# Performance work log

Hardware: AMD Instinct MI355X
Metric: run time of the kernel (lower is better)

The kernel has to match this reference:

```python
import jax, jax.numpy as jnp
import numpy as np

EPS = float(np.finfo(np.float32).eps)
FFT_SIZE, HOP, WIN = 1024, 120, 600
ANCHOR, KF = 7, 7
LRELU_SLOPE = 0.1

def make_log_shift(anchor=ANCHOR, kf=KF, out_scale=1000.0, in_scale=0.001):
    s = (np.arange(kf) + 1) / anchor
    ls = out_scale * np.log(in_scale * s)
    ls -= ls[anchor - 1]
    return -ls  # positive, monotonically decreasing to 0 at the anchor tap

SHIFTS = make_log_shift()

def stft_mag(y):
    # y: (B, T) -> (B, 513, n_frames), matches torch.stft(center=True, reflect)
    B, T = y.shape
    pad = FFT_SIZE // 2
    yp = jnp.pad(y, ((0, 0), (pad, pad)), mode='reflect')
    n_frames = 1 + (T + 2 * pad - FFT_SIZE) // HOP
    idx = jnp.arange(n_frames)[:, None] * HOP + jnp.arange(FFT_SIZE)[None, :]
    frames = yp[:, idx]                                  # (B, n_frames, fft)
    n = np.arange(WIN)
    w = 0.5 * (1.0 - np.cos(2.0 * np.pi * n / WIN))      # periodic Hann(600)
    lp = (FFT_SIZE - WIN) // 2                           # centered pad to fft
    w = jnp.asarray(np.pad(w, (lp, FFT_SIZE - WIN - lp)), dtype=y.dtype)
    spec = jnp.fft.rfft(frames * w, axis=-1)
    mag = jnp.sqrt(jnp.clip(spec.real ** 2 + spec.imag ** 2, EPS))
    return jnp.transpose(mag, (0, 2, 1))

def int_shift(x, k):
    # output[..., f, :] = x[..., f-k, :], zero-fill; k >= 0 (static python int)
    F = x.shape[2]
    if k == 0:
        return x
    if k >= F:
        return jnp.zeros_like(x)
    return jnp.pad(x[:, :, :F - k, :], ((0, 0), (0, 0), (k, 0), (0, 0)))

def frac_shift(x, s):
    # linear-interpolation frequency shift (= interp_shift CUDA kernel)
    if s == int(s):
        return int_shift(x, int(s))
    s0 = int(np.floor(s)); frac = float(s - s0)
    return (1.0 - frac) * int_shift(x, s0) + frac * int_shift(x, s0 + 1)

def wnorm(v, g):
    # weight_norm: w = g * v / ||v|| (norm over all dims but out-channel)
    n = jnp.sqrt(jnp.sum(v * v, axis=(1, 2, 3), keepdims=True))
    return g * v / n

def conv2d(x, w, b, stride, padding):
    out = jax.lax.conv_general_dilated(
        x, w, window_strides=stride,
        padding=((padding[0], padding[0]), (padding[1], padding[1])),
        dimension_numbers=('NCHW', 'OIHW', 'NCHW'))
    return out + b[None, :, None, None]

def lrelu(x):
    return jax.nn.leaky_relu(x, LRELU_SLOPE)

def harmonic_conv(x, v, g, b):
    # x: (B,1,F,T). Log-harmonic lowering: stack 7 fractionally-shifted copies
    lowered = jnp.concatenate([frac_shift(x, SHIFTS[fk]) for fk in range(KF)], axis=1)
    w = wnorm(v, g)                                      # (32, 7, 1, 7)
    return conv2d(lowered, w, b, (1, 1), (0, 3))         # padding[0] forced to 0

def setup_inputs() -> dict:
    key = jax.random.key(0)
    ks = jax.random.split(key, 16)
    p = {}
    p['y'] = jax.random.normal(ks[0], (4, 1, 96000), dtype=jnp.float32)
    p['v0'] = jax.random.normal(ks[1], (32, 7, 1, 7), dtype=jnp.float32) * 0.05
    p['g0'] = jnp.ones((32, 1, 1, 1), dtype=jnp.float32)
    p['b0'] = jnp.zeros((32,), dtype=jnp.float32)
    for i, kk in zip((1, 2, 3), (2, 3, 4)):
        p[f'v{i}'] = jax.random.normal(ks[kk], (32, 32, 3, 9), dtype=jnp.float32) * 0.05
        p[f'g{i}'] = jnp.ones((32, 1, 1, 1), dtype=jnp.float32)
        p[f'b{i}'] = jnp.zeros((32,), dtype=jnp.float32)
    p['v4'] = jax.random.normal(ks[5], (32, 32, 3, 3), dtype=jnp.float32) * 0.05
    p['g4'] = jnp.ones((32, 1, 1, 1), dtype=jnp.float32)
    p['b4'] = jnp.zeros((32,), dtype=jnp.float32)
    p['vo'] = jax.random.normal(ks[6], (1, 32, 3, 3), dtype=jnp.float32) * 0.05
    p['go'] = jnp.ones((1, 1, 1, 1), dtype=jnp.float32)
    p['bo'] = jnp.zeros((1,), dtype=jnp.float32)
    return p

def reference(y, v0, g0, b0, v1, g1, b1, v2, g2, b2, v3, g3, b3,
              v4, g4, b4, vo, go, bo):
    mag = stft_mag(y[:, 0, :])          # (B, 513, frames)
    x = mag[:, None]                    # (B, 1, 513, frames)
    fmap = []
    x = lrelu(harmonic_conv(x, v0, g0, b0)); fmap.append(x)
    x = lrelu(conv2d(x, wnorm(v1, g1), b1, (1, 2), (1, 4))); fmap.append(x)
    x = lrelu(conv2d(x, wnorm(v2, g2), b2, (1, 2), (1, 4))); fmap.append(x)
    x = lrelu(conv2d(x, wnorm(v3, g3), b3, (1, 2), (1, 4))); fmap.append(x)
    x = lrelu(conv2d(x, wnorm(v4, g4), b4, (1, 1), (1, 1))); fmap.append(x)
    x = conv2d(x, wnorm(vo, go), bo, (1, 1), (1, 1)); fmap.append(x)
    flat = x.reshape(x.shape[0], -1)
    return (flat,) + tuple(fmap)
```

## Files before the change

kernel.cpp:

```cpp
#include <hip/hip_runtime.h>
#include <math.h>

#define T_SAMPLES 96000
#define NFRAMES 801
#define NBINS 513
#define FROWS 515
#define MAGT 804
#define EPS32 1.1920928955078125e-07f

typedef _Float16 f16;
typedef f16 f16x2 __attribute__((ext_vector_type(2)));
typedef f16 f16x4 __attribute__((ext_vector_type(4)));
typedef f16 f16x8 __attribute__((ext_vector_type(8)));
typedef float f32x4 __attribute__((ext_vector_type(4)));
typedef float f32x16 __attribute__((ext_vector_type(16)));

__global__ __launch_bounds__(256) void stft_v2(const float* __restrict__ y,
                                               float* __restrict__ mag)
{
    __shared__ float2 fft[2][4][1024];
    float* mg = (float*)&fft[1][0][0];
    const int MGS = 520;

    const int tid  = threadIdx.x;
    const int lane = tid & 63;
    const int wv   = tid >> 6;
    const int t0   = blockIdx.x * 8;
    const int b    = blockIdx.y;
    const float* yb = y + (size_t)b * T_SAMPLES;

    const int tA = t0 + 2 * wv;
    for (int n = lane; n < 1024; n += 64) {
        float w = 0.f;
        int np_ = n - 212;
        if (np_ >= 0 && np_ < 600)
            w = 0.5f * (1.0f - cospif((float)np_ * (1.0f / 300.0f)));
        int j1 = tA * 120 + n - 512;
        if (j1 < 0) j1 = -j1;
        if (j1 >= T_SAMPLES) j1 = 2 * T_SAMPLES - 2 - j1;
        int j2 = j1 + 120;
        {
            int jj = tA * 120 + 120 + n - 512;
            if (jj < 0) jj = -jj;
            if (jj >= T_SAMPLES) jj = 2 * T_SAMPLES - 2 - jj;
            j2 = jj;
        }
        fft[0][wv][n] = make_float2(w * yb[j1], w * yb[j2]);
    }
    __syncthreads();

    int srcb = 0;
    #pragma unroll
    for (int stage = 0; stage < 10; ++stage) {
        int m = 1 << stage;
        #pragma unroll
        for (int it = 0; it < 8; ++it) {
            int idx = lane + it * 64;
            int jm  = (idx >> stage) << stage;
            float jf = (float)jm * (1.0f / 512.0f);
            float wr = cospif(jf);
            float wi = -sinpif(jf);
            float2 a  = fft[srcb][wv][idx];
            float2 bb = fft[srcb][wv][idx + 512];
            float2 s  = make_float2(a.x + bb.x, a.y + bb.y);
            float2 d  = make_float2(a.x - bb.x, a.y - bb.y);
            float2 dw = make_float2(d.x * wr - d.y * wi, d.x * wi + d.y * wr);
            fft[srcb ^ 1][wv][idx + jm]     = s;
            fft[srcb ^ 1][wv][idx + jm + m] = dw;
        }
        __syncthreads();
        srcb ^= 1;
    }

    for (int k = lane; k < 513; k += 64) {
        float2 zk = fft[0][wv][k];
        float2 zr = fft[0][wv][(1024 - k) & 1023];
        float x1r = 0.5f * (zk.x + zr.x);
        float x1i = 0.5f * (zk.y - zr.y);
        float x2r = 0.5f * (zk.y + zr.y);
        float x2i = 0.5f * (zr.x - zk.x);
        mg[(2 * wv)     * MGS + k] = sqrtf(fmaxf(x1r * x1r + x1i * x1i, EPS32));
        mg[(2 * wv + 1) * MGS + k] = sqrtf(fmaxf(x2r * x2r + x2i * x2i, EPS32));
    }
    __syncthreads();

    for (int f = tid; f < 513; f += 256) {
        size_t base = ((size_t)(b * NBINS) + f) * MAGT + t0;
        if (t0 + 7 < NFRAMES) {
            f32x4 v0 = {mg[0 * MGS + f], mg[1 * MGS + f], mg[2 * MGS + f], mg[3 * MGS + f]};
            f32x4 v1 = {mg[4 * MGS + f], mg[5 * MGS + f], mg[6 * MGS + f], mg[7 * MGS + f]};
            *reinterpret_cast<f32x4*>(&mag[base])     = v0;
            *reinterpret_cast<f32x4*>(&mag[base + 4]) = v1;
        } else {
            #pragma unroll
            for (int p = 0; p < 8; ++p)
                if (t0 + p < NFRAMES) mag[base + p] = mg[p * MGS + f];
        }
    }
}

__global__ __launch_bounds__(256) void prep_kernel(
    const float* __restrict__ v0, const float* __restrict__ g0,
    const float* __restrict__ v1, const float* __restrict__ g1,
    const float* __restrict__ v2, const float* __restrict__ g2,
    const float* __restrict__ v3, const float* __restrict__ g3,
    const float* __restrict__ v4, const float* __restrict__ g4,
    const float* __restrict__ vo, const float* __restrict__ go,
    float* __restrict__ w0n, float* __restrict__ won,
    f16* __restrict__ A1, f16* __restrict__ A2,
    f16* __restrict__ A3, f16* __restrict__ A4,
    f16* __restrict__ f0c, f16* __restrict__ f1c, f16* __restrict__ f2c,
    f16* __restrict__ f3c, f16* __restrict__ f4c)
{
    int blk = blockIdx.x;
    int tid = threadIdx.x;

    if (blk >= 161) {
        int zb = blk - 161;
        const int TPs[5]   = {840, 456, 264, 136, 136};
        const int tails[5] = {840, 420, 228, 133, 136};
        f16* ptrs[5] = {f0c, f1c, f2c, f3c, f4c};
        f16x8 z;
        #pragma unroll
        for (int j = 0; j < 8; ++j) z[j] = (f16)0.f;
        for (int l = 0; l < 5; ++l) {
            f16* p = ptrs[l];
            int TP = TPs[l], tail = tails[l];
            int rowSlots   = TP * 4;
            int guardSlots = 8 * rowSlots;
            int tailCols   = TP - tail;
            int tailSlots  = 4 * FROWS * tailCols * 4;
            int total = guardSlots + tailSlots;
            for (int i = zb * 256 + tid; i < total; i += 256 * 256) {
                size_t slot;
                if (i < guardSlots) {
                    int rs = i / rowSlots;
                    int q  = i - rs * rowSlots;
                    int b  = rs >> 1;
                    int r  = (rs & 1) ? (FROWS - 1) : 0;
                    slot = ((size_t)(b * FROWS + r)) * rowSlots + q;
                } else {
                    int j2 = i - guardSlots;
                    int per = tailCols * 4;
                    int row = j2 / per;
                    int q   = j2 - row * per;
                    slot = ((size_t)row * TP + tail) * 4 + q;
                }
                *reinterpret_cast<f16x8*>((char*)p + slot * 16) = z;
            }
        }
        return;
    }

    const float *v, *g; f16* Ap = nullptr; float* outf = nullptr;
    int o, per_o, KW = 9;
    if (blk < 32)        { v = v1; g = g1; Ap = A1; o = blk;       per_o = 864; }
    else if (blk < 64)   { v = v2; g = g2; Ap = A2; o = blk - 32;  per_o = 864; }
    else if (blk < 96)   { v = v3; g = g3; Ap = A3; o = blk - 64;  per_o = 864; }
    else if (blk < 128)  { v = v4; g = g4; Ap = A4; o = blk - 96;  per_o = 288; KW = 3; }
    else if (blk < 160)  { v = v0; g = g0; outf = w0n; o = blk - 128; per_o = 49; }
    else                 { v = vo; g = go; outf = won; o = 0;        per_o = 288; }

    const float* vv = v + (size_t)o * per_o;
    __shared__ float red[256];
    float s = 0.f;
    for (int i = tid; i < per_o; i += 256) { float x = vv[i]; s = fmaf(x, x, s); }
    red[tid] = s;
    __syncthreads();
    for (int k = 128; k > 0; k >>= 1) {
        if (tid < k) red[tid] += red[tid + k];
        __syncthreads();
    }
    float scale = g[o] / sqrtf(red[0]);

    if (outf) {
        for (int i = tid; i < per_o; i += 256)
            outf[(size_t)o * per_o + i] = vv[i] * scale;
    } else {
        for (int i = tid; i < per_o; i += 256) {
            int tap = i >> 5;
            int c   = i & 31;
            int df  = tap / KW, kw = tap - df * KW;
            float val = vv[(c * 3 + df) * KW + kw] * scale;
            int l = ((c >> 3) & 1) * 32 + o;
            int ch = c >> 4;
            int j = c & 7;
            Ap[(((tap * 2 + ch) * 64 + l) << 3) + j] = (f16)val;
        }
    }
}

__global__ __launch_bounds__(256) void harmonic_kernel(const float* __restrict__ mag,
                                                       const float* __restrict__ wn,
                                                       const float* __restrict__ bias,
                                                       float* __restrict__ out,
                                                       f16* __restrict__ f0c,
                                                       float fr4, float fr5)
{
    int f = blockIdx.x;
    int b = blockIdx.y;
    int tid = threadIdx.x;

    __shared__ float rows[3][808];

    const float* mb = mag + (size_t)b * NBINS * MAGT;

    for (int i = tid; i < 808; i += 256) {
        int tt = i - 3;
        bool ok = (tt >= 0) && (tt < NFRAMES);
        float m336 = (ok && f >= 336) ? mb[(size_t)(f - 336) * MAGT + tt] : 0.f;
        float m337 = (ok && f >= 337) ? mb[(size_t)(f - 337) * MAGT + tt] : 0.f;
        float m154 = (ok && f >= 154) ? mb[(size_t)(f - 154) * MAGT + tt] : 0.f;
        float m155 = (ok && f >= 155) ? mb[(size_t)(f - 155) * MAGT + tt] : 0.f;
        float m0   = ok ? mb[(size_t)f * MAGT + tt] : 0.f;
        rows[0][i] = (1.f - fr4) * m336 + fr4 * m337;
        rows[1][i] = (1.f - fr5) * m154 + fr5 * m155;
        rows[2][i] = m0;
    }
    __syncthreads();

    char* crow = (char*)f0c + ((size_t)(b * FROWS + f + 1)) * 840 * 64;

    if (tid < 16) {
        int tg = tid >> 2, q = tid & 3;
        int swz = (((tg >> 1) & 3) << 4) | (((tg >> 3) & 1) << 6);
        f16x8 z;
        #pragma unroll
        for (int j = 0; j < 8; ++j) z[j] = (f16)0.f;
        *reinterpret_cast<f16x8*>(crow + ((tg * 64 + q * 16) ^ swz)) = z;
    }

    #pragma unroll
    for (int chunk = 0; chunk < 4; ++chunk) {
        int t = chunk * 256 + tid;
        if (t < NFRAMES) {
            float win[3][7];
            #pragma unroll
            for (int r = 0; r < 3; ++r)
                #pragma unroll
                for (int k = 0; k < 7; ++k)
                    win[r][k] = rows[r][t + k];

            float vals[32];
            #pragma unroll
            for (int o = 0; o < 32; ++o) {
                float a = bias[o];
                #pragma unroll
                for (int r = 0; r < 3; ++r) {
                    const float* wr = wn + (o * 7 + 4 + r) * 7;
                    #pragma unroll
                    for (int kw = 0; kw < 7; ++kw)
                        a = fmaf(win[r][kw], wr[kw], a);
                }
                vals[o] = (a > 0.f) ? a : 0.1f * a;
            }

            #pragma unroll
            for (int o = 0; o < 32; ++o)
                out[(((size_t)b * 32 + o) * NBINS + f) * (size_t)NFRAMES + t] = vals[o];

            int tg = t + 4;
            int swz = (((tg >> 1) & 3) << 4) | (((tg >> 3) & 1) << 6);
            #pragma unroll
            for (int q = 0; q < 4; ++q) {
                f16x8 h;
                #pragma unroll
                for (int j = 0; j < 8; ++j) h[j] = (f16)vals[q * 8 + j];
                *reinterpret_cast<f16x8*>(crow + ((tg * 64 + q * 16) ^ swz)) = h;
            }
        } else if (t < 836) {
            int tg = t + 4;
            int swz = (((tg >> 1) & 3) << 4) | (((tg >> 3) & 1) << 6);
            f16x8 z;
            #pragma unroll
            for (int j = 0; j < 8; ++j) z[j] = (f16)0.f;
            #pragma unroll
            for (int q = 0; q < 4; ++q)
                *reinterpret_cast<f16x8*>(crow + ((tg * 64 + q * 16) ^ swz)) = z;
        }
    }
}

template<int KW, int STRIDE, int PW, int PAD_IN, int PAD_OUT, int NTB, int MINW, bool DO_LRELU>
__global__ __launch_bounds__(256, MINW) void conv_v6(
    const f16* __restrict__ inC, const f16* __restrict__ Ap,
    const float* __restrict__ bias, float* __restrict__ out,
    f16* __restrict__ outC, int Tout, int TpadIn, int TpadOut)
{
    constexpr int NT    = 64;
    constexpr int TR    = NT * STRIDE + KW - 1;
    constexpr int TRP   = (TR + 1) & ~1;
    constexpr int ROWB  = TRP * 64;
    constexpr int SLR   = TRP * 4;
    constexpr int SL    = 6 * SLR;
    constexpr int KPT   = (SL + 255) / 256;
    constexpr int TOFF  = (PAD_IN - PW) & 15;
    constexpr int NFOFF = 32 * STRIDE * 64;

    __shared__ char ldsb[KPT * 256 * 16];

    const int tid  = threadIdx.x;
    const int lane = tid & 63;
    const int wave = tid >> 6;

    const int NWG = NTB * 129 * 4;
    int lin = blockIdx.x;
    int xcd = lin & 7, sl = lin >> 3;
    const int q = NWG / 8, r = NWG % 8;
    int work = (xcd < r ? xcd * (q + 1) : r * (q + 1) + (xcd - r) * q) + sl;
    const int tb   = work % NTB;
    int rem        = work / NTB;
    const int fblk = rem % 129;
    const int b    = rem / 129;
    const int f0   = fblk * 4;
    const int brow = b * FROWS + f0;
    const int t0   = tb * NT;
    const int base_t = t0 * STRIDE + (PAD_IN - PW);

    {
        const char* inB = (const char*)inC;
        #pragma unroll
        for (int k = 0; k < KPT; ++k) {
            int s  = tid + k * 256;
            int fr = s / SLR;
            int s2 = s - fr * SLR;
            __builtin_amdgcn_global_load_lds(
                (const __attribute__((address_space(1))) void*)
                    (inB + ((size_t)(brow + fr) * TpadIn + base_t) * 64 + (size_t)s2 * 16),
                (__attribute__((address_space(3))) void*)
                    (ldsb + (k * 256 + (tid & 192)) * 16),
                16, 0, 0);
        }
    }

    const int tln = lane & 31;
    const int hi  = lane >> 5;
    int baddr0[KW];
    #pragma unroll
    for (int kw = 0; kw < KW; ++kw) {
        int trow = tln * STRIDE + kw;
        int x = trow + TOFF;
        int swz = (((x >> 1) & 3) << 4) | (((x >> 3) & 1) << 6);
        baddr0[kw] = (trow * 64 + hi * 16) ^ swz;
    }

    float bs[16];
    #pragma unroll
    for (int rr = 0; rr < 16; ++rr) bs[rr] = bias[4 * hi + 8 * (rr >> 2) + (rr & 3)];

    __syncthreads();

    f32x16 acc[2];
    #pragma unroll
    for (int nf = 0; nf < 2; ++nf)
        #pragma unroll
        for (int rr = 0; rr < 16; ++rr) acc[nf][rr] = 0.f;

    const char* lrow = ldsb + wave * ROWB;
    #pragma unroll
    for (int df = 0; df < 3; ++df) {
        f16x8 a[KW * 2];
        #pragma unroll
        for (int kw = 0; kw < KW; ++kw)
            #pragma unroll
            for (int ch = 0; ch < 2; ++ch)
                a[kw * 2 + ch] = *reinterpret_cast<const f16x8*>(
                    Ap + (((df * KW + kw) * 2 + ch) << 9) + lane * 8);
        #pragma unroll
        for (int kw = 0; kw < KW; ++kw)
            #pragma unroll
            for (int ch = 0; ch < 2; ++ch)
                #pragma unroll
                for (int nf = 0; nf < 2; ++nf) {
                    f16x8 bf = *reinterpret_cast<const f16x8*>(
                        lrow + ((baddr0[kw] ^ (ch << 5)) + df * ROWB + nf * NFOFF));
                    acc[nf] = __builtin_amdgcn_mfma_f32_32x32x16_f16(a[kw * 2 + ch], bf, acc[nf], 0, 0, 0);
                }
    }

    const int f = f0 + wave;
    if (f >= NBINS) return;

    char* crow = nullptr;
    if constexpr (PAD_OUT > 0)
        crow = (char*)outC + ((size_t)(b * FROWS + f + 1)) * TpadOut * 64;

    #pragma unroll
    for (int nf = 0; nf < 2; ++nf) {
        int t = t0 + nf * 32 + tln;
        bool vt = (t < Tout);
        float vals[16];
        #pragma unroll
        for (int rr = 0; rr < 16; ++rr) {
            float v = acc[nf][rr] + bs[rr];
            if (DO_LRELU) v = (v > 0.f) ? v : 0.1f * v;
            vals[rr] = v;
        }
        if (vt) {
            #pragma unroll
            for (int rr = 0; rr < 16; ++rr) {
                int o = 4 * hi + 8 * (rr >> 2) + (rr & 3);
                out[(((size_t)b * 32 + o) * NBINS + f) * Tout + t] = vals[rr];
            }
        }
        if constexpr (PAD_OUT > 0) {
            int tg = t + PAD_OUT;
            int swz = (((tg >> 1) & 3) << 4) | (((tg >> 3) & 1) << 6);
            int rowbyte = (tg * 64) ^ swz;
            #pragma unroll
            for (int qq = 0; qq < 4; ++qq) {
                f16x4 hv;
                #pragma unroll
                for (int rr = 0; rr < 4; ++rr)
                    hv[rr] = vt ? (f16)vals[4 * qq + rr] : (f16)0.f;
                *reinterpret_cast<f16x4*>(crow + (rowbyte ^ ((4 * hi + 8 * qq) << 1))) = hv;
            }
        }
    }
    if constexpr (PAD_OUT > 0) {
        if (tb == 0 && lane < PAD_OUT * 4) {
            int tgp = lane >> 2, oct = lane & 3;
            f16x8 z;
            #pragma unroll
            for (int j = 0; j < 8; ++j) z[j] = (f16)0.f;
            *reinterpret_cast<f16x8*>(crow + tgp * 64 + oct * 16) = z;
        }
    }
}

__global__ __launch_bounds__(256) void convo_v2(const f16* __restrict__ inC,
                                                const float* __restrict__ won,
                                                const float* __restrict__ bias,
                                                float* __restrict__ f5,
                                                float* __restrict__ flat)
{
    const int TP4 = 136;
    int blk = blockIdx.x;
    int b = blk / 257, fp = blk - (b * 257);
    int tid = threadIdx.x;
    int f = fp * 2 + (tid >> 7);
    int t = tid & 127;
    if (f >= NBINS || t >= 101) return;

    float acc = bias[0];
    #pragma unroll
    for (int df = 0; df < 3; ++df) {
        const char* row = (const char*)inC + ((size_t)(b * FROWS + f + df)) * TP4 * 64;
        #pragma unroll
        for (int kw = 0; kw < 3; ++kw) {
            int tg = t + kw;
            int swz = (((tg >> 1) & 3) << 4) | (((tg >> 3) & 1) << 6);
            #pragma unroll
            for (int q2 = 0; q2 < 4; ++q2) {
                f16x8 h = *reinterpret_cast<const f16x8*>(row + ((tg * 64 + q2 * 16) ^ swz));
                #pragma unroll
                for (int j = 0; j < 8; ++j)
                    acc = fmaf((float)h[j], won[((q2 * 8 + j) * 3 + df) * 3 + kw], acc);
            }
        }
    }
    size_t idx = ((size_t)(b * NBINS + f)) * 101 + t;
    f5[idx] = acc;
    flat[idx] = acc;
}

extern "C" void kernel_launch(void* const* d_in, const int* in_sizes, int n_in,
                              void* d_out, int out_size, void* d_ws, size_t ws_size,
                              hipStream_t stream)
{
    const float* y  = (const float*)d_in[0];
    const float* v0 = (const float*)d_in[1];
    const float* g0 = (const float*)d_in[2];
    const float* b0 = (const float*)d_in[3];
    const float* v1 = (const float*)d_in[4];
    const float* g1 = (const float*)d_in[5];
    const float* b1 = (const float*)d_in[6];
    const float* v2 = (const float*)d_in[7];
    const float* g2 = (const float*)d_in[8];
    const float* b2 = (const float*)d_in[9];
    const float* v3 = (const float*)d_in[10];
    const float* g3 = (const float*)d_in[11];
    const float* b3 = (const float*)d_in[12];
    const float* v4 = (const float*)d_in[13];
    const float* g4 = (const float*)d_in[14];
    const float* b4 = (const float*)d_in[15];
    const float* vo = (const float*)d_in[16];
    const float* go = (const float*)d_in[17];
    const float* bo = (const float*)d_in[18];

    float* out = (float*)d_out;
    float* ws  = (float*)d_ws;

    const size_t SFLAT = (size_t)4 * NBINS * 101;
    const size_t NF0   = (size_t)4 * 32 * NBINS * 801;
    const size_t NF1   = (size_t)4 * 32 * NBINS * 401;
    const size_t NF2   = (size_t)4 * 32 * NBINS * 201;
    const size_t NF3   = (size_t)4 * 32 * NBINS * 101;
    float* oflat = out;
    float* f0 = out + SFLAT;
    float* f1 = f0 + NF0;
    float* f2 = f1 + NF1;
    float* f3 = f2 + NF2;
    float* f4 = f3 + NF3;
    float* f5 = f4 + NF3;

    float* mag = f1;

    const int TP0 = 840, TP1 = 456, TP2 = 264, TP3 = 136, TP4 = 136;
    size_t off = 0;
    float* w0n = ws + off; off += 1568;
    float* won = ws + off; off += 288;
    f16* A1 = (f16*)(ws + off);
    f16* A2 = A1 + 27648;
    f16* A3 = A2 + 27648;
    f16* A4 = A3 + 27648;
    f16* f0c = A4 + 9216;
    f16* f1c = f0c + (size_t)4 * FROWS * TP0 * 32;
    f16* f2c = f1c + (size_t)4 * FROWS * TP1 * 32;
    f16* f3c = f2c + (size_t)4 * FROWS * TP2 * 32;
    f16* f4c = f3c + (size_t)4 * FROWS * TP3 * 32;

    prep_kernel<<<417, 256, 0, stream>>>(v0, g0, v1, g1, v2, g2, v3, g3,
                                         v4, g4, vo, go, w0n, won,
                                         A1, A2, A3, A4,
                                         f0c, f1c, f2c, f3c, f4c);

    stft_v2<<<dim3(101, 4), 256, 0, stream>>>(y, mag);

    double sh4 = -(1000.0 * log(0.001 * (5.0 / 7.0)) - 1000.0 * log(0.001));
    double sh5 = -(1000.0 * log(0.001 * (6.0 / 7.0)) - 1000.0 * log(0.001));
    float fr4 = (float)(sh4 - floor(sh4));
    float fr5 = (float)(sh5 - floor(sh5));

    harmonic_kernel<<<dim3(NBINS, 4), 256, 0, stream>>>(mag, w0n, b0, f0, f0c, fr4, fr5);

    conv_v6<9, 2, 4, 4, 4, 7, 3, true><<<7 * 129 * 4, 256, 0, stream>>>(f0c, A1, b1, f1, f1c, 401, TP0, TP1);
    conv_v6<9, 2, 4, 4, 4, 4, 3, true><<<4 * 129 * 4, 256, 0, stream>>>(f1c, A2, b2, f2, f2c, 201, TP1, TP2);
    conv_v6<9, 2, 4, 4, 5, 2, 3, true><<<2 * 129 * 4, 256, 0, stream>>>(f2c, A3, b3, f3, f3c, 101, TP2, TP3);
    conv_v6<3, 1, 1, 5, 1, 2, 4, true><<<2 * 129 * 4, 256, 0, stream>>>(f3c, A4, b4, f4, f4c, 101, TP3, TP4);

    convo_v2<<<257 * 4, 256, 0, stream>>>(f4c, won, bo, f5, oflat);
}
```

Before: 392.6 us.

## Merge STFT into prep kernel and use nontemporal stores for fmap outputs

Result: slower. 410.5 us (+4.6%).

```diff
diff --git a/kernel.cpp b/kernel.cpp
--- a/kernel.cpp
+++ b/kernel.cpp
@@ -15,91 +15,8 @@
 typedef float f32x4 __attribute__((ext_vector_type(4)));
 typedef float f32x16 __attribute__((ext_vector_type(16)));
 
-__global__ __launch_bounds__(256) void stft_v2(const float* __restrict__ y,
-                                               float* __restrict__ mag)
-{
-    __shared__ float2 fft[2][4][1024];
-    float* mg = (float*)&fft[1][0][0];
-    const int MGS = 520;
-
-    const int tid  = threadIdx.x;
-    const int lane = tid & 63;
-    const int wv   = tid >> 6;
-    const int t0   = blockIdx.x * 8;
-    const int b    = blockIdx.y;
-    const float* yb = y + (size_t)b * T_SAMPLES;
-
-    const int tA = t0 + 2 * wv;
-    for (int n = lane; n < 1024; n += 64) {
-        float w = 0.f;
-        int np_ = n - 212;
-        if (np_ >= 0 && np_ < 600)
-            w = 0.5f * (1.0f - cospif((float)np_ * (1.0f / 300.0f)));
-        int j1 = tA * 120 + n - 512;
-        if (j1 < 0) j1 = -j1;
-        if (j1 >= T_SAMPLES) j1 = 2 * T_SAMPLES - 2 - j1;
-        int j2 = j1 + 120;
-        {
-            int jj = tA * 120 + 120 + n - 512;
-            if (jj < 0) jj = -jj;
-            if (jj >= T_SAMPLES) jj = 2 * T_SAMPLES - 2 - jj;
-            j2 = jj;
-        }
-        fft[0][wv][n] = make_float2(w * yb[j1], w * yb[j2]);
-    }
-    __syncthreads();
-
-    int srcb = 0;
-    #pragma unroll
-    for (int stage = 0; stage < 10; ++stage) {
-        int m = 1 << stage;
-        #pragma unroll
-        for (int it = 0; it < 8; ++it) {
-            int idx = lane + it * 64;
-            int jm  = (idx >> stage) << stage;
-            float jf = (float)jm * (1.0f / 512.0f);
-            float wr = cospif(jf);
-            float wi = -sinpif(jf);
-            float2 a  = fft[srcb][wv][idx];
-            float2 bb = fft[srcb][wv][idx + 512];
-            float2 s  = make_float2(a.x + bb.x, a.y + bb.y);
-            float2 d  = make_float2(a.x - bb.x, a.y - bb.y);
-            float2 dw = make_float2(d.x * wr - d.y * wi, d.x * wi + d.y * wr);
-            fft[srcb ^ 1][wv][idx + jm]     = s;
-            fft[srcb ^ 1][wv][idx + jm + m] = dw;
-        }
-        __syncthreads();
-        srcb ^= 1;
-    }
-
-    for (int k = lane; k < 513; k += 64) {
-        float2 zk = fft[0][wv][k];
-        float2 zr = fft[0][wv][(1024 - k) & 1023];
-        float x1r = 0.5f * (zk.x + zr.x);
-        float x1i = 0.5f * (zk.y - zr.y);
-        float x2r = 0.5f * (zk.y + zr.y);
-        float x2i = 0.5f * (zr.x - zk.x);
-        mg[(2 * wv)     * MGS + k] = sqrtf(fmaxf(x1r * x1r + x1i * x1i, EPS32));
-        mg[(2 * wv + 1) * MGS + k] = sqrtf(fmaxf(x2r * x2r + x2i * x2i, EPS32));
-    }
-    __syncthreads();
-
-    for (int f = tid; f < 513; f += 256) {
-        size_t base = ((size_t)(b * NBINS) + f) * MAGT + t0;
-        if (t0 + 7 < NFRAMES) {
-            f32x4 v0 = {mg[0 * MGS + f], mg[1 * MGS + f], mg[2 * MGS + f], mg[3 * MGS + f]};
-            f32x4 v1 = {mg[4 * MGS + f], mg[5 * MGS + f], mg[6 * MGS + f], mg[7 * MGS + f]};
-            *reinterpret_cast<f32x4*>(&mag[base])     = v0;
-            *reinterpret_cast<f32x4*>(&mag[base + 4]) = v1;
-        } else {
-            #pragma unroll
-            for (int p = 0; p < 8; ++p)
-                if (t0 + p < NFRAMES) mag[base + p] = mg[p * MGS + f];
-        }
-    }
-}
-
-__global__ __launch_bounds__(256) void prep_kernel(
+__global__ __launch_bounds__(256) void prep_stft_kernel(
+    const float* __restrict__ y, float* __restrict__ mag,
     const float* __restrict__ v0, const float* __restrict__ g0,
     const float* __restrict__ v1, const float* __restrict__ g1,
     const float* __restrict__ v2, const float* __restrict__ g2,
@@ -112,8 +29,90 @@
     f16* __restrict__ f0c, f16* __restrict__ f1c, f16* __restrict__ f2c,
     f16* __restrict__ f3c, f16* __restrict__ f4c)
 {
+    __shared__ float2 fbuf[2][1024];
+    __shared__ float mg[8][520];
+    const int MGS = 520;
+
     int blk = blockIdx.x;
     int tid = threadIdx.x;
+
+    if (blk >= 417) {
+        int s = blk - 417;
+        int b = s / 101;
+        int t0 = (s - b * 101) * 8;
+        const float* yb = y + (size_t)b * T_SAMPLES;
+
+        #pragma unroll 1
+        for (int pp = 0; pp < 4; ++pp) {
+            int tA = t0 + 2 * pp;
+            #pragma unroll
+            for (int it = 0; it < 4; ++it) {
+                int n = tid + it * 256;
+                float w = 0.f;
+                int np_ = n - 212;
+                if (np_ >= 0 && np_ < 600)
+                    w = 0.5f * (1.0f - cospif((float)np_ * (1.0f / 300.0f)));
+                int j1 = tA * 120 + n - 512;
+                if (j1 < 0) j1 = -j1;
+                if (j1 >= T_SAMPLES) j1 = 2 * T_SAMPLES - 2 - j1;
+                int j2 = tA * 120 + 120 + n - 512;
+                if (j2 < 0) j2 = -j2;
+                if (j2 >= T_SAMPLES) j2 = 2 * T_SAMPLES - 2 - j2;
+                fbuf[0][n] = make_float2(w * yb[j1], w * yb[j2]);
+            }
+            __syncthreads();
+
+            int srcb = 0;
+            #pragma unroll
+            for (int stage = 0; stage < 10; ++stage) {
+                int m = 1 << stage;
+                #pragma unroll
+                for (int it = 0; it < 2; ++it) {
+                    int idx = tid + it * 256;
+                    int jm  = (idx >> stage) << stage;
+                    float jf = (float)jm * (1.0f / 512.0f);
+                    float wr = cospif(jf);
+                    float wi = -sinpif(jf);
+                    float2 a  = fbuf[srcb][idx];
+                    float2 bb = fbuf[srcb][idx + 512];
+                    float2 sm = make_float2(a.x + bb.x, a.y + bb.y);
+                    float2 d  = make_float2(a.x - bb.x, a.y - bb.y);
+                    float2 dw = make_float2(d.x * wr - d.y * wi, d.x * wi + d.y * wr);
+                    fbuf[srcb ^ 1][idx + jm]     = sm;
+                    fbuf[srcb ^ 1][idx + jm + m] = dw;
+                }
+                __syncthreads();
+                srcb ^= 1;
+            }
+
+            for (int k = tid; k < 513; k += 256) {
+                float2 zk = fbuf[0][k];
+                float2 zr = fbuf[0][(1024 - k) & 1023];
+                float x1r = 0.5f * (zk.x + zr.x);
+                float x1i = 0.5f * (zk.y - zr.y);
+                float x2r = 0.5f * (zk.y + zr.y);
+                float x2i = 0.5f * (zr.x - zk.x);
+                mg[2 * pp][k]     = sqrtf(fmaxf(x1r * x1r + x1i * x1i, EPS32));
+                mg[2 * pp + 1][k] = sqrtf(fmaxf(x2r * x2r + x2i * x2i, EPS32));
+            }
+            __syncthreads();
+        }
+
+        for (int f = tid; f < 513; f += 256) {
+            size_t base = ((size_t)(b * NBINS) + f) * MAGT + t0;
+            if (t0 + 7 < NFRAMES) {
+                f32x4 q0 = {mg[0][f], mg[1][f], mg[2][f], mg[3][f]};
+                f32x4 q1 = {mg[4][f], mg[5][f], mg[6][f], mg[7][f]};
+                *reinterpret_cast<f32x4*>(&mag[base])     = q0;
+                *reinterpret_cast<f32x4*>(&mag[base + 4]) = q1;
+            } else {
+                #pragma unroll
+                for (int p = 0; p < 8; ++p)
+                    if (t0 + p < NFRAMES) mag[base + p] = mg[p][f];
+            }
+        }
+        return;
+    }
 
     if (blk >= 161) {
         int zb = blk - 161;
@@ -161,8 +160,8 @@
     else if (blk < 160)  { v = v0; g = g0; outf = w0n; o = blk - 128; per_o = 49; }
     else                 { v = vo; g = go; outf = won; o = 0;        per_o = 288; }
 
+    float* red = (float*)&fbuf[0][0];
     const float* vv = v + (size_t)o * per_o;
-    __shared__ float red[256];
     float s = 0.f;
     for (int i = tid; i < per_o; i += 256) { float x = vv[i]; s = fmaf(x, x, s); }
     red[tid] = s;
@@ -257,7 +256,8 @@
 
             #pragma unroll
             for (int o = 0; o < 32; ++o)
-                out[(((size_t)b * 32 + o) * NBINS + f) * (size_t)NFRAMES + t] = vals[o];
+                __builtin_nontemporal_store(vals[o],
+                    &out[(((size_t)b * 32 + o) * NBINS + f) * (size_t)NFRAMES + t]);
 
             int tg = t + 4;
             int swz = (((tg >> 1) & 3) << 4) | (((tg >> 3) & 1) << 6);
@@ -400,7 +400,8 @@
             #pragma unroll
             for (int rr = 0; rr < 16; ++rr) {
                 int o = 4 * hi + 8 * (rr >> 2) + (rr & 3);
-                out[(((size_t)b * 32 + o) * NBINS + f) * Tout + t] = vals[rr];
+                __builtin_nontemporal_store(vals[rr],
+                    &out[(((size_t)b * 32 + o) * NBINS + f) * Tout + t]);
             }
         }
         if constexpr (PAD_OUT > 0) {
@@ -460,8 +461,8 @@
         }
     }
     size_t idx = ((size_t)(b * NBINS + f)) * 101 + t;
-    f5[idx] = acc;
-    flat[idx] = acc;
+    __builtin_nontemporal_store(acc, &f5[idx]);
+    __builtin_nontemporal_store(acc, &flat[idx]);
 }
 
 extern "C" void kernel_launch(void* const* d_in, const int* in_sizes, int n_in,
@@ -520,12 +521,11 @@
     f16* f3c = f2c + (size_t)4 * FROWS * TP2 * 32;
     f16* f4c = f3c + (size_t)4 * FROWS * TP3 * 32;
 
-    prep_kernel<<<417, 256, 0, stream>>>(v0, g0, v1, g1, v2, g2, v3, g3,
-                                         v4, g4, vo, go, w0n, won,
-                                         A1, A2, A3, A4,
-                                         f0c, f1c, f2c, f3c, f4c);
-
-    stft_v2<<<dim3(101, 4), 256, 0, stream>>>(y, mag);
+    prep_stft_kernel<<<821, 256, 0, stream>>>(y, mag,
+                                              v0, g0, v1, g1, v2, g2, v3, g3,
+                                              v4, g4, vo, go, w0n, won,
+                                              A1, A2, A3, A4,
+                                              f0c, f1c, f2c, f3c, f4c);
 
     double sh4 = -(1000.0 * log(0.001 * (5.0 / 7.0)) - 1000.0 * log(0.001));
     double sh5 = -(1000.0 * log(0.001 * (6.0 / 7.0)) - 1000.0 * log(0.001));
```
